# Kernel optimization log

Hardware: AMD Instinct MI355X
Metric: run time of the kernel (lower is better)

The kernel has to match this reference:

```python
import jax, jax.numpy as jnp
import numpy as np

B, NUM, LENTH, AUX = 32, 64, 64, 64
SIZE, OUT = 256, 256
IN_G = (LENTH + 1) * 2 + AUX  # 194


def _linear_params(k, fan_in, fan_out):
    # torch nn.Linear default init: U(-1/sqrt(fan_in), 1/sqrt(fan_in))
    s = 1.0 / np.sqrt(fan_in)
    kw, kb = jax.random.split(k)
    W = jax.random.uniform(kw, (fan_in, fan_out), minval=-s, maxval=s, dtype=jnp.float32)
    b = jax.random.uniform(kb, (fan_out,), minval=-s, maxval=s, dtype=jnp.float32)
    return W, b


def setup_inputs() -> dict:
    key = jax.random.key(0)
    ks = jax.random.split(key, 8)
    inp = {"x_aux": jax.random.normal(ks[0], (B, NUM, LENTH + AUX), dtype=jnp.float32)}
    dims = [("g1", IN_G, SIZE), ("g2", SIZE, SIZE), ("g3", SIZE, SIZE), ("g4", SIZE, OUT),
            ("f1", OUT, SIZE), ("f2", SIZE, SIZE), ("f3", SIZE, OUT)]
    for k, (name, fi, fo) in zip(ks[1:], dims):
        W, b = _linear_params(k, fi, fo)
        inp[name + "_w"] = W
        inp[name + "_b"] = b
    return inp


def reference(x_aux, g1_w, g1_b, g2_w, g2_b, g3_w, g3_b, g4_w, g4_b,
              f1_w, f1_b, f2_w, f2_b, f3_w, f3_b):
    bsz = x_aux.shape[0]
    # coord feature = object index i
    coord = jnp.broadcast_to(
        jnp.arange(NUM, dtype=x_aux.dtype)[None, :, None], (bsz, NUM, 1))
    x = jnp.concatenate([x_aux[:, :, :LENTH], coord], axis=-1)      # [B, N, LENTH+1]
    xa = jnp.concatenate([x_aux, coord], axis=-1)                   # [B, N, LENTH+AUX+1]
    # all-pairs broadcast+concat -> [B, N, N, IN_G]
    x_i = jnp.broadcast_to(x[:, None, :, :], (bsz, NUM, NUM, LENTH + 1))
    x_j = jnp.broadcast_to(xa[:, :, None, :], (bsz, NUM, NUM, LENTH + AUX + 1))
    pairs = jnp.concatenate([x_i, x_j], axis=-1)
    # shared g-MLP over every pair
    h = jax.nn.relu(pairs @ g1_w + g1_b)
    h = jax.nn.relu(h @ g2_w + g2_b)
    h = jax.nn.relu(h @ g3_w + g3_b)
    h = jax.nn.relu(h @ g4_w + g4_b)
    # sum-pool over all N*N pairs -> [B, OUT]
    x_g = h.sum(axis=(1, 2))
    # f-MLP (dropout treated as identity / eval mode)
    x_f = jax.nn.relu(x_g @ f1_w + f1_b)
    x_f = jax.nn.relu(x_f @ f2_w + f2_b)
    return x_f @ f3_w + f3_b
```

## Files before the change

kernel.cpp:

```cpp
#include <hip/hip_runtime.h>

#define BATCH 32
#define NOBJ  64
#define PADK  264

typedef _Float16 f16x2 __attribute__((ext_vector_type(2)));
typedef __fp16   h16x2 __attribute__((ext_vector_type(2)));
typedef _Float16 f16x4 __attribute__((ext_vector_type(4)));
typedef _Float16 f16x8 __attribute__((ext_vector_type(8)));
typedef float    f32x4 __attribute__((ext_vector_type(4)));
typedef float    f32x16 __attribute__((ext_vector_type(16)));

#define MFMA32(a, b, c) __builtin_amdgcn_mfma_f32_32x32x16_f16((a), (b), (c), 0, 0, 0)


__global__ __launch_bounds__(256) void prep_all(
    const float* __restrict__ x_aux,
    const float* __restrict__ g1w, const float* __restrict__ g1b,
    const float* __restrict__ g2w, const float* __restrict__ g3w,
    const float* __restrict__ g4w,
    _Float16* __restrict__ wtf, float* __restrict__ xg,
    float* __restrict__ cib, float* __restrict__ h0j) {
  __shared__ _Float16 tile[256][33];
  const int blk = blockIdx.x;
  const int t = threadIdx.x;

  if (blk < 32) {
    xg[blk * 256 + t] = 0.0f;
    const int l = blk >> 3;
    if (l == 0) return;
    const int nt = blk & 7;
    const float* src = (l == 1) ? g2w : (l == 2) ? g3w : g4w;

    const int nn = t & 31, kb = t >> 5;
#pragma unroll 4
    for (int pass = 0; pass < 32; ++pass) {
      int kp = pass * 8 + kb;
      int kl = (l == 1) ? kp
                        : 64 * (kp >> 6) + 32 * (kp & 1) + ((kp & 63) >> 1);
      tile[kp][nn] = (_Float16)src[(size_t)kl * 256 + nt * 32 + nn];
    }
    __syncthreads();

    const int lane = t & 63;
    const int nfrag = lane & 31;
    const int kbase = (lane >> 5) * 8;
    _Float16* dst = wtf + ((size_t)(l * 8 + nt) * 16) * 512;
#pragma unroll
    for (int q = 0; q < 4; ++q) {
      int kk = (t >> 6) + 4 * q;
      f16x8 fr;
#pragma unroll
      for (int j = 0; j < 8; ++j)
        fr[j] = tile[kk * 16 + kbase + j][nfrag];
      *(f16x8*)(dst + (size_t)kk * 512 + lane * 8) = fr;
    }
  } else if (blk < 544) {
    float* xs = (float*)&tile[0][0];
    const int blkc = blk - 32;
    const int b  = blkc >> 4;
    const int i0 = (blkc & 15) * 4;

#pragma unroll
    for (int u = 0; u < 2; ++u) {
      int idx = u * 256 + t;
      int j = idx >> 7, k = idx & 127;
      xs[j * 128 + k] = x_aux[((size_t)(b * NOBJ + i0 + j)) * 128 + k];
    }
    __syncthreads();

    float c0 = 0.f, c1 = 0.f, c2 = 0.f, c3 = 0.f;
#pragma unroll 8
    for (int k = 0; k < 128; ++k) {
      float w = g1w[(size_t)(65 + k) * 256 + t];
      c0 += xs[k] * w;       c1 += xs[128 + k] * w;
      c2 += xs[256 + k] * w; c3 += xs[384 + k] * w;
    }
    float wc = g1w[(size_t)193 * 256 + t];
    float bb = g1b[t];
    c0 += (float)(i0 + 0) * wc + bb;
    c1 += (float)(i0 + 1) * wc + bb;
    c2 += (float)(i0 + 2) * wc + bb;
    c3 += (float)(i0 + 3) * wc + bb;
    cib[((size_t)(b * NOBJ + i0 + 0)) * 256 + t] = c0;
    cib[((size_t)(b * NOBJ + i0 + 1)) * 256 + t] = c1;
    cib[((size_t)(b * NOBJ + i0 + 2)) * 256 + t] = c2;
    cib[((size_t)(b * NOBJ + i0 + 3)) * 256 + t] = c3;
  } else {
    float* xs = (float*)&tile[0][0];
    const int blk2 = blk - 544;
    const int b  = blk2 >> 3;
    const int j0 = (blk2 & 7) * 8;

#pragma unroll
    for (int u = 0; u < 2; ++u) {
      int idx = u * 256 + t;
      int jj = idx >> 6, k = idx & 63;
      xs[jj * 65 + k] = x_aux[((size_t)(b * NOBJ + j0 + jj)) * 128 + k];
    }
    if (t < 8) xs[t * 65 + 64] = (float)(j0 + t);
    __syncthreads();

    float acc[8] = {};
#pragma unroll 5
    for (int k = 0; k < 65; ++k) {
      float w = g1w[(size_t)k * 256 + t];
#pragma unroll
      for (int jj = 0; jj < 8; ++jj) acc[jj] += xs[jj * 65 + k] * w;
    }
#pragma unroll
    for (int jj = 0; jj < 8; ++jj)
      h0j[((size_t)(b * NOBJ + j0 + jj)) * 256 + t] = acc[jj];
  }
}

__device__ __forceinline__ void do_layer16(
    const _Float16* __restrict__ bp0, const _Float16* __restrict__ bp1,
    const _Float16* __restrict__ arow, f32x16 acc[8]) {
#pragma unroll
  for (int kk = 0; kk < 16; ++kk) {
    f16x8 b0 = *(const f16x8*)(bp0 + (size_t)kk * 512);
    f16x8 b1 = *(const f16x8*)(bp1 + (size_t)kk * 512);
#pragma unroll
    for (int m = 0; m < 4; ++m) {
      f16x8 a = *(const f16x8*)(arow + (size_t)m * 32 * PADK + kk * 16);
      acc[m * 2]     = MFMA32(a, b0, acc[m * 2]);
      acc[m * 2 + 1] = MFMA32(a, b1, acc[m * 2 + 1]);
    }
  }
}

__global__ __launch_bounds__(256, 2) void g_mlp_pool(
    const float* __restrict__ h0j,
    const float* __restrict__ cib,
    const _Float16* __restrict__ wtf,
    const float* __restrict__ g2b, const float* __restrict__ g3b,
    const float* __restrict__ g4b,
    float* __restrict__ xg) {
  __shared__ _Float16 As[128][PADK];

  const int b  = blockIdx.x >> 5;
  const int i0 = (blockIdx.x & 31) * 2;
  const int t  = threadIdx.x;
  const int lane = t & 63;
  const int wv   = t >> 6;

  {
    const int c = lane * 4;
    const float* hb = h0j + (size_t)(b * NOBJ) * 256 + c;
    const float* c0p = cib + (size_t)(b * NOBJ + i0) * 256 + c;
    f32x4 cv0 = *(const f32x4*)c0p;
    f32x4 cv1 = *(const f32x4*)(c0p + 256);
#pragma unroll
    for (int it = 0; it < 16; ++it) {
      int j = it * 4 + wv;
      f32x4 hv = *(const f32x4*)(hb + (size_t)j * 256);
      f16x4 p0, p1;
#pragma unroll
      for (int q = 0; q < 4; ++q) {
        p0[q] = (_Float16)fmaxf(hv[q] + cv0[q], 0.f);
        p1[q] = (_Float16)fmaxf(hv[q] + cv1[q], 0.f);
      }
      *(f16x4*)&As[j][c]      = p0;
      *(f16x4*)&As[64 + j][c] = p1;
    }
  }
  __syncthreads();

  const int nq   = wv;
  const int c31  = lane & 31;
  const int h    = lane >> 5;
  const int n0   = nq * 64;
  const float* gb[4] = {nullptr, g2b, g3b, g4b};

  for (int layer = 1; layer < 4; ++layer) {
    const float bv0 = gb[layer][n0 + c31];
    const float bv1 = gb[layer][n0 + 32 + c31];

    f32x16 acc[8];
#pragma unroll
    for (int x = 0; x < 8; ++x) acc[x] = (f32x16){};

    const _Float16* bp0 =
        wtf + ((size_t)(layer * 8 + nq * 2) * 16) * 512 + lane * 8;
    const _Float16* bp1 = bp0 + 16 * 512;
    const _Float16* arow = &As[c31][h * 8];

    do_layer16(bp0, bp1, arow, acc);

    if (layer < 3) {
      __syncthreads();
#pragma unroll
      for (int m = 0; m < 4; ++m)
#pragma unroll
        for (int g = 0; g < 4; ++g)
#pragma unroll
          for (int r = 0; r < 4; ++r) {
            const int row = m * 32 + g * 8 + h * 4 + r;
            const int reg = g * 4 + r;
            h16x2 pk = __builtin_amdgcn_cvt_pkrtz(
                fmaxf(acc[m * 2][reg] + bv0, 0.f),
                fmaxf(acc[m * 2 + 1][reg] + bv1, 0.f));
            *(h16x2*)&As[row][n0 + 2 * c31] = pk;
          }
      __syncthreads();
    } else {
      float s0 = 0.f, s1 = 0.f;
#pragma unroll
      for (int m = 0; m < 4; ++m)
#pragma unroll
        for (int reg = 0; reg < 16; ++reg) {
          s0 += fmaxf(acc[m * 2][reg] + bv0, 0.f);
          s1 += fmaxf(acc[m * 2 + 1][reg] + bv1, 0.f);
        }
      s0 += __shfl_xor(s0, 32, 64);
      s1 += __shfl_xor(s1, 32, 64);
      if (h == 0) {
        atomicAdd(&xg[b * 256 + n0 + c31], s0);
        atomicAdd(&xg[b * 256 + n0 + 32 + c31], s1);
      }
    }
  }
}

__global__ __launch_bounds__(1024) void f_mlp(
    const float* __restrict__ xg,
    const float* __restrict__ f1w, const float* __restrict__ f1b,
    const float* __restrict__ f2w, const float* __restrict__ f2b,
    const float* __restrict__ f3w, const float* __restrict__ f3b,
    float* __restrict__ out) {
  __shared__ float xs[256], ys[256], ps[4][256];
  const int b = blockIdx.x;
  const int t = threadIdx.x;
  const int n = t & 255;
  const int kc = t >> 8;

  if (t < 256) xs[t] = xg[b * 256 + t];
  __syncthreads();

  float p = 0.f;
#pragma unroll 8
  for (int k0 = 0; k0 < 64; ++k0) {
    int k = kc * 64 + k0;
    p += xs[k] * f1w[k * 256 + n];
  }
  ps[kc][n] = p;
  __syncthreads();
  if (t < 256)
    ys[t] = fmaxf(f1b[t] + ps[0][t] + ps[1][t] + ps[2][t] + ps[3][t], 0.f);
  __syncthreads();

  p = 0.f;
#pragma unroll 8
  for (int k0 = 0; k0 < 64; ++k0) {
    int k = kc * 64 + k0;
    p += ys[k] * f2w[k * 256 + n];
  }
  ps[kc][n] = p;
  __syncthreads();
  if (t < 256)
    xs[t] = fmaxf(f2b[t] + ps[0][t] + ps[1][t] + ps[2][t] + ps[3][t], 0.f);
  __syncthreads();

  p = 0.f;
#pragma unroll 8
  for (int k0 = 0; k0 < 64; ++k0) {
    int k = kc * 64 + k0;
    p += xs[k] * f3w[k * 256 + n];
  }
  ps[kc][n] = p;
  __syncthreads();
  if (t < 256)
    out[b * 256 + t] = f3b[t] + ps[0][t] + ps[1][t] + ps[2][t] + ps[3][t];
}

extern "C" void kernel_launch(void* const* d_in, const int* in_sizes, int n_in,
                              void* d_out, int out_size, void* d_ws, size_t ws_size,
                              hipStream_t stream) {
  const float* x_aux = (const float*)d_in[0];
  const float* g1w = (const float*)d_in[1];
  const float* g1b = (const float*)d_in[2];
  const float* g2w = (const float*)d_in[3];
  const float* g2b = (const float*)d_in[4];
  const float* g3w = (const float*)d_in[5];
  const float* g3b = (const float*)d_in[6];
  const float* g4w = (const float*)d_in[7];
  const float* g4b = (const float*)d_in[8];
  const float* f1w = (const float*)d_in[9];
  const float* f1b = (const float*)d_in[10];
  const float* f2w = (const float*)d_in[11];
  const float* f2b = (const float*)d_in[12];
  const float* f3w = (const float*)d_in[13];
  const float* f3b = (const float*)d_in[14];
  float* out = (float*)d_out;

  _Float16* wtf = (_Float16*)d_ws;
  float* xg  = (float*)((char*)d_ws + 512u * 1024u);
  float* cib = (float*)((char*)d_ws + 544u * 1024u);
  float* h0j = (float*)((char*)d_ws + 544u * 1024u + 2048u * 1024u);

  hipLaunchKernelGGL(prep_all, dim3(800), dim3(256), 0, stream,
                     x_aux, g1w, g1b, g2w, g3w, g4w, wtf, xg, cib, h0j);
  hipLaunchKernelGGL(g_mlp_pool, dim3(BATCH * 32), dim3(256), 0, stream,
                     h0j, cib, wtf, g2b, g3b, g4b, xg);
  hipLaunchKernelGGL(f_mlp, dim3(BATCH), dim3(1024), 0, stream,
                     xg, f1w, f1b, f2w, f2b, f3w, f3b, out);
}
```

Before: 148.4 us.

## Split g-MLP block work across 8 waves and vectorize prep LDS reads

```diff
diff --git a/kernel.cpp b/kernel.cpp
--- a/kernel.cpp
+++ b/kernel.cpp
@@ -21,7 +21,7 @@
     const float* __restrict__ g4w,
     _Float16* __restrict__ wtf, float* __restrict__ xg,
     float* __restrict__ cib, float* __restrict__ h0j) {
-  __shared__ _Float16 tile[256][33];
+  __shared__ __align__(16) _Float16 tile[256][33];
   const int blk = blockIdx.x;
   const int t = threadIdx.x;
 
@@ -70,11 +70,18 @@
     __syncthreads();
 
     float c0 = 0.f, c1 = 0.f, c2 = 0.f, c3 = 0.f;
-#pragma unroll 8
-    for (int k = 0; k < 128; ++k) {
-      float w = g1w[(size_t)(65 + k) * 256 + t];
-      c0 += xs[k] * w;       c1 += xs[128 + k] * w;
-      c2 += xs[256 + k] * w; c3 += xs[384 + k] * w;
+#pragma unroll 2
+    for (int k = 0; k < 128; k += 4) {
+      f32x4 x0 = *(const f32x4*)&xs[k];
+      f32x4 x1 = *(const f32x4*)&xs[128 + k];
+      f32x4 x2 = *(const f32x4*)&xs[256 + k];
+      f32x4 x3 = *(const f32x4*)&xs[384 + k];
+#pragma unroll
+      for (int q = 0; q < 4; ++q) {
+        float w = g1w[(size_t)(65 + k + q) * 256 + t];
+        c0 += x0[q] * w; c1 += x1[q] * w;
+        c2 += x2[q] * w; c3 += x3[q] * w;
+      }
     }
     float wc = g1w[(size_t)193 * 256 + t];
     float bb = g1b[t];
@@ -96,33 +103,41 @@
     for (int u = 0; u < 2; ++u) {
       int idx = u * 256 + t;
       int jj = idx >> 6, k = idx & 63;
-      xs[jj * 65 + k] = x_aux[((size_t)(b * NOBJ + j0 + jj)) * 128 + k];
-    }
-    if (t < 8) xs[t * 65 + 64] = (float)(j0 + t);
+      xs[jj * 68 + k] = x_aux[((size_t)(b * NOBJ + j0 + jj)) * 128 + k];
+    }
     __syncthreads();
 
     float acc[8] = {};
-#pragma unroll 5
-    for (int k = 0; k < 65; ++k) {
-      float w = g1w[(size_t)k * 256 + t];
-#pragma unroll
-      for (int jj = 0; jj < 8; ++jj) acc[jj] += xs[jj * 65 + k] * w;
-    }
+#pragma unroll 2
+    for (int k = 0; k < 64; k += 4) {
+      f32x4 xv[8];
+#pragma unroll
+      for (int jj = 0; jj < 8; ++jj)
+        xv[jj] = *(const f32x4*)&xs[jj * 68 + k];
+#pragma unroll
+      for (int q = 0; q < 4; ++q) {
+        float w = g1w[(size_t)(k + q) * 256 + t];
+#pragma unroll
+        for (int jj = 0; jj < 8; ++jj) acc[jj] += xv[jj][q] * w;
+      }
+    }
+    float wc = g1w[(size_t)64 * 256 + t];
 #pragma unroll
     for (int jj = 0; jj < 8; ++jj)
-      h0j[((size_t)(b * NOBJ + j0 + jj)) * 256 + t] = acc[jj];
+      h0j[((size_t)(b * NOBJ + j0 + jj)) * 256 + t] =
+          acc[jj] + (float)(j0 + jj) * wc;
   }
 }
 
 __device__ __forceinline__ void do_layer16(
     const _Float16* __restrict__ bp0, const _Float16* __restrict__ bp1,
-    const _Float16* __restrict__ arow, f32x16 acc[8]) {
+    const _Float16* __restrict__ arow, f32x16 acc[4]) {
 #pragma unroll
   for (int kk = 0; kk < 16; ++kk) {
     f16x8 b0 = *(const f16x8*)(bp0 + (size_t)kk * 512);
     f16x8 b1 = *(const f16x8*)(bp1 + (size_t)kk * 512);
 #pragma unroll
-    for (int m = 0; m < 4; ++m) {
+    for (int m = 0; m < 2; ++m) {
       f16x8 a = *(const f16x8*)(arow + (size_t)m * 32 * PADK + kk * 16);
       acc[m * 2]     = MFMA32(a, b0, acc[m * 2]);
       acc[m * 2 + 1] = MFMA32(a, b1, acc[m * 2 + 1]);
@@ -130,14 +145,14 @@
   }
 }
 
-__global__ __launch_bounds__(256, 2) void g_mlp_pool(
+__global__ __launch_bounds__(512, 4) void g_mlp_pool(
     const float* __restrict__ h0j,
     const float* __restrict__ cib,
     const _Float16* __restrict__ wtf,
     const float* __restrict__ g2b, const float* __restrict__ g3b,
     const float* __restrict__ g4b,
     float* __restrict__ xg) {
-  __shared__ _Float16 As[128][PADK];
+  __shared__ __align__(16) _Float16 As[128][PADK];
 
   const int b  = blockIdx.x >> 5;
   const int i0 = (blockIdx.x & 31) * 2;
@@ -152,8 +167,8 @@
     f32x4 cv0 = *(const f32x4*)c0p;
     f32x4 cv1 = *(const f32x4*)(c0p + 256);
 #pragma unroll
-    for (int it = 0; it < 16; ++it) {
-      int j = it * 4 + wv;
+    for (int it = 0; it < 8; ++it) {
+      int j = it * 8 + wv;
       f32x4 hv = *(const f32x4*)(hb + (size_t)j * 256);
       f16x4 p0, p1;
 #pragma unroll
@@ -167,7 +182,8 @@
   }
   __syncthreads();
 
-  const int nq   = wv;
+  const int nq   = wv & 3;
+  const int mh   = wv >> 2;
   const int c31  = lane & 31;
   const int h    = lane >> 5;
   const int n0   = nq * 64;
@@ -177,26 +193,26 @@
     const float bv0 = gb[layer][n0 + c31];
     const float bv1 = gb[layer][n0 + 32 + c31];
 
-    f32x16 acc[8];
-#pragma unroll
-    for (int x = 0; x < 8; ++x) acc[x] = (f32x16){};
+    f32x16 acc[4];
+#pragma unroll
+    for (int x = 0; x < 4; ++x) acc[x] = (f32x16){};
 
     const _Float16* bp0 =
         wtf + ((size_t)(layer * 8 + nq * 2) * 16) * 512 + lane * 8;
     const _Float16* bp1 = bp0 + 16 * 512;
-    const _Float16* arow = &As[c31][h * 8];
+    const _Float16* arow = &As[c31][h * 8] + (size_t)mh * 64 * PADK;
 
     do_layer16(bp0, bp1, arow, acc);
 
     if (layer < 3) {
       __syncthreads();
 #pragma unroll
-      for (int m = 0; m < 4; ++m)
+      for (int m = 0; m < 2; ++m)
 #pragma unroll
         for (int g = 0; g < 4; ++g)
 #pragma unroll
           for (int r = 0; r < 4; ++r) {
-            const int row = m * 32 + g * 8 + h * 4 + r;
+            const int row = (mh * 2 + m) * 32 + g * 8 + h * 4 + r;
             const int reg = g * 4 + r;
             h16x2 pk = __builtin_amdgcn_cvt_pkrtz(
                 fmaxf(acc[m * 2][reg] + bv0, 0.f),
@@ -207,7 +223,7 @@
     } else {
       float s0 = 0.f, s1 = 0.f;
 #pragma unroll
-      for (int m = 0; m < 4; ++m)
+      for (int m = 0; m < 2; ++m)
 #pragma unroll
         for (int reg = 0; reg < 16; ++reg) {
           s0 += fmaxf(acc[m * 2][reg] + bv0, 0.f);
@@ -301,7 +317,7 @@
 
   hipLaunchKernelGGL(prep_all, dim3(800), dim3(256), 0, stream,
                      x_aux, g1w, g1b, g2w, g3w, g4w, wtf, xg, cib, h0j);
-  hipLaunchKernelGGL(g_mlp_pool, dim3(BATCH * 32), dim3(256), 0, stream,
+  hipLaunchKernelGGL(g_mlp_pool, dim3(BATCH * 32), dim3(512), 0, stream,
                      h0j, cib, wtf, g2b, g3b, g4b, xg);
   hipLaunchKernelGGL(f_mlp, dim3(BATCH), dim3(1024), 0, stream,
                      xg, f1w, f1b, f2w, f2b, f3w, f3b, out);
```

After: 152.8 us. +3.0%, slower.
